# Kernel tuning notes

Measured on AMD Instinct MI355X. Metric: run time of the kernel, lower is better.

The kernel has to match this reference:

```python
import jax, jax.numpy as jnp
import numpy as np

Q, N, D = 4096, 100000, 128


def setup_inputs() -> dict:
    key = jax.random.key(0)
    k1, k2, k3 = jax.random.split(key, 3)
    inputs = jax.random.normal(k1, (Q, D), dtype=jnp.float32)
    X_train = jax.random.normal(k2, (N, D), dtype=jnp.float32)
    y_train = jax.random.normal(k3, (N,), dtype=jnp.float32)
    return {"inputs": inputs, "X_train": X_train, "y_train": y_train, "k": 32}


def reference(inputs, X_train, y_train, k):
    # Squared Euclidean distances [Q, N] via the expanded identity
    # |a-b|^2 = |a|^2 + |b|^2 - 2 a.b  (avoids materializing [Q, N, D]).
    q_sq = jnp.sum(inputs * inputs, axis=-1, keepdims=True)        # [Q, 1]
    t_sq = jnp.sum(X_train * X_train, axis=-1)                     # [N]
    cross = jnp.einsum('qd,nd->qn', inputs, X_train)               # [Q, N]
    distances = q_sq + t_sq[None, :] - 2.0 * cross                 # [Q, N]
    # top_k of -distances == k nearest neighbors
    _, indices = jax.lax.top_k(-distances, k)                      # [Q, k]
    nearest = y_train[indices]                                     # [Q, k]
    return jnp.mean(nearest, axis=1)                               # [Q]
```

## Files before the change

kernel.cpp:

```cpp
#include <hip/hip_runtime.h>
#include <hip/hip_fp16.h>
#include <cstdint>
#include <cstddef>


constexpr int Q_  = 4096;
constexpr int N_  = 100000;
constexpr int D_  = 128;
constexpr int K_  = 32;

constexpr int QT    = 16;
constexpr int BN    = 256;
constexpr int NCH   = 8;
constexpr int CHUNK = 12544;
constexpr int ITERS = CHUNK / BN;
constexpr int NPAD  = NCH * CHUNK;
constexpr int CW    = 128;
constexpr int QTS   = 16;
constexpr int SAMP_M      = 8192;
constexpr int SAMP_STRIDE = 12;
constexpr int SAMP_OFF    = 5;
constexpr int SAMP_ITERS  = SAMP_M / BN;

constexpr int XS_B  = NPAD / 64;
constexpr int SAM_B = SAMP_M / 64;
constexpr int PQ_B  = Q_ / 4;
constexpr int MXN   = XS_B * 4;

typedef __attribute__((ext_vector_type(8))) _Float16 half8;
typedef __attribute__((ext_vector_type(4))) float    floatx4;
typedef unsigned long long ull;

#define DEV __device__ __forceinline__
constexpr ull DEADC = ~0ull;

DEV ull pack_cand(float score, unsigned int n) {
    unsigned int s = __float_as_uint(score);
    s = (s & 0x80000000u) ? ~s : (s | 0x80000000u);
    return ((ull)s << 32) | (ull)n;
}
DEV float unpack_score(ull k) {
    unsigned int s = (unsigned int)(k >> 32);
    s = (s & 0x80000000u) ? (s ^ 0x80000000u) : ~s;
    return __uint_as_float(s);
}
DEV ull u64min(ull a, ull b) { return a < b ? a : b; }
DEV float inf_f() { return __int_as_float(0x7f800000); }

DEV ull bitonic64(ull v, int L) {
    #pragma unroll
    for (int k2 = 2; k2 <= 64; k2 <<= 1)
        #pragma unroll
        for (int j2 = k2 >> 1; j2 >= 1; j2 >>= 1) {
            ull o = __shfl_xor(v, j2);
            bool up = ((L & k2) == 0);
            bool lo = ((L & j2) == 0);
            ull mn = u64min(v, o), mx = v ^ o ^ mn;
            v = (lo == up) ? mn : mx;
        }
    return v;
}
DEV ull bimerge64(ull v, int L) {
    #pragma unroll
    for (int j2 = 32; j2 >= 1; j2 >>= 1) {
        ull o = __shfl_xor(v, j2);
        ull mn = u64min(v, o), mx = v ^ o ^ mn;
        v = ((L & j2) == 0) ? mn : mx;
    }
    return v;
}

__global__ void prep_all(const float* __restrict__ X, const float* __restrict__ Qm,
                         __half* __restrict__ Xs, float* __restrict__ tsq,
                         float* __restrict__ mxArr,
                         __half* __restrict__ Xsam, float* __restrict__ tsqS,
                         __half* __restrict__ Qh, __half* __restrict__ Qr,
                         float* __restrict__ qsq, int* __restrict__ flagF)
{
    const int tid = threadIdx.x, L = tid & 63, wv = tid >> 6;
    const int bx = blockIdx.x;
    const int am = L & 15, aq = L >> 4;

    if (bx < XS_B) {
        int t16 = bx * 4 + wv;
        int r = t16 * 16 + am;
        float ssq = 0.f, xr2 = 0.f;
        #pragma unroll
        for (int ks = 0; ks < 4; ++ks) {
            int c = ks * 32 + aq * 8;
            float v0=0,v1=0,v2=0,v3=0,v4=0,v5=0,v6=0,v7=0;
            if (r < N_) {
                float4 a = *(const float4*)(X + (size_t)r * D_ + c);
                float4 b = *(const float4*)(X + (size_t)r * D_ + c + 4);
                v0=a.x; v1=a.y; v2=a.z; v3=a.w; v4=b.x; v5=b.y; v6=b.z; v7=b.w;
            }
            half8 h;
            h[0]=(_Float16)v0; h[1]=(_Float16)v1; h[2]=(_Float16)v2; h[3]=(_Float16)v3;
            h[4]=(_Float16)v4; h[5]=(_Float16)v5; h[6]=(_Float16)v6; h[7]=(_Float16)v7;
            float r0=v0-(float)h[0], r1=v1-(float)h[1], r2=v2-(float)h[2], r3=v3-(float)h[3];
            float r4=v4-(float)h[4], r5=v5-(float)h[5], r6=v6-(float)h[6], r7=v7-(float)h[7];
            ssq += v0*v0+v1*v1+v2*v2+v3*v3+v4*v4+v5*v5+v6*v6+v7*v7;
            xr2 += r0*r0+r1*r1+r2*r2+r3*r3+r4*r4+r5*r5+r6*r6+r7*r7;
            *(half8*)(Xs + ((size_t)(t16 * 4 + ks)) * 512 + L * 8) = h;
        }
        ssq += __shfl_xor(ssq, 16); ssq += __shfl_xor(ssq, 32);
        xr2 += __shfl_xor(xr2, 16); xr2 += __shfl_xor(xr2, 32);
        if (aq == 0) tsq[r] = (r < N_) ? ssq : inf_f();
        float m = xr2;
        m = fmaxf(m, __shfl_xor(m, 1)); m = fmaxf(m, __shfl_xor(m, 2));
        m = fmaxf(m, __shfl_xor(m, 4)); m = fmaxf(m, __shfl_xor(m, 8));
        if (L == 0) mxArr[t16] = m;
    } else if (bx < XS_B + SAM_B) {
        int t16 = (bx - XS_B) * 4 + wv;
        int j = t16 * 16 + am;
        int n = j * SAMP_STRIDE + SAMP_OFF;
        float ssq = 0.f;
        #pragma unroll
        for (int ks = 0; ks < 4; ++ks) {
            int c = ks * 32 + aq * 8;
            float4 a = *(const float4*)(X + (size_t)n * D_ + c);
            float4 b = *(const float4*)(X + (size_t)n * D_ + c + 4);
            half8 h;
            h[0]=(_Float16)a.x; h[1]=(_Float16)a.y; h[2]=(_Float16)a.z; h[3]=(_Float16)a.w;
            h[4]=(_Float16)b.x; h[5]=(_Float16)b.y; h[6]=(_Float16)b.z; h[7]=(_Float16)b.w;
            ssq += a.x*a.x + a.y*a.y + a.z*a.z + a.w*a.w
                 + b.x*b.x + b.y*b.y + b.z*b.z + b.w*b.w;
            *(half8*)(Xsam + ((size_t)(t16 * 4 + ks)) * 512 + L * 8) = h;
        }
        ssq += __shfl_xor(ssq, 16); ssq += __shfl_xor(ssq, 32);
        if (aq == 0) tsqS[j] = ssq;
    } else {
        int r = (bx - XS_B - SAM_B) * 4 + wv;
        float2 x = *(const float2*)(Qm + (size_t)r * D_ + 2 * L);
        __half h0 = __float2half(x.x), h1 = __float2half(x.y);
        size_t o = (size_t)r * D_ + 2 * L;
        Qh[o] = h0; Qh[o + 1] = h1;
        Qr[o]     = __float2half(x.x - __half2float(h0));
        Qr[o + 1] = __float2half(x.y - __half2float(h1));
        float s = x.x * x.x + x.y * x.y;
        s += __shfl_xor(s, 32); s += __shfl_xor(s, 16); s += __shfl_xor(s, 8);
        s += __shfl_xor(s, 4);  s += __shfl_xor(s, 2);  s += __shfl_xor(s, 1);
        if (L == 0) { qsq[r] = s; flagF[r] = 0; }
    }
}

__global__ __launch_bounds__(256, 2) void sample_T(
    const __half* __restrict__ Qh, const __half* __restrict__ Qr,
    const __half* __restrict__ Xsam, const float* __restrict__ tsqS,
    const float* __restrict__ qsq, const float* __restrict__ mxArr,
    float* __restrict__ Teff, float* __restrict__ rawT, float* __restrict__ EwA)
{
    __shared__ float sT[QTS][130];
    const int tid = threadIdx.x, L = tid & 63, wv = tid >> 6;
    const int qbase = blockIdx.x * QTS;
    const int nwv = wv * 64;
    const int am = L & 15, aq = L >> 4;

    half8 afh[4], afr[4];
    #pragma unroll
    for (int ks = 0; ks < 4; ++ks) {
        size_t o = (size_t)(qbase + am) * D_ + ks * 32 + aq * 8;
        afh[ks] = *(const half8*)(Qh + o);
        afr[ks] = *(const half8*)(Qr + o);
    }

    float t2a[4], t2b[4];
    #pragma unroll
    for (int rg = 0; rg < 4; ++rg) { t2a[rg] = inf_f(); t2b[rg] = inf_f(); }

    const __half* bp = Xsam + (size_t)nwv * 128 + (size_t)L * 8;
    const float*  tp = tsqS + nwv + am;

    half8 bc[4], bn[4];
    #pragma unroll
    for (int nt = 0; nt < 4; ++nt)
        bc[nt] = *(const half8*)(bp + nt * 2048);

    #pragma unroll 1
    for (int it = 0; it < SAMP_ITERS; ++it) {
        float ts[4];
        #pragma unroll
        for (int nt = 0; nt < 4; ++nt) ts[nt] = tp[nt * 16];

        floatx4 acc[4] = {};
        #pragma unroll
        for (int ks = 0; ks < 4; ++ks) {
            const __half* pp = (ks < 3) ? (bp + (ks + 1) * 512) : (bp + 32768);
            #pragma unroll
            for (int nt = 0; nt < 4; ++nt)
                bn[nt] = *(const half8*)(pp + nt * 2048);
            #pragma unroll
            for (int nt = 0; nt < 4; ++nt) {
                acc[nt] = __builtin_amdgcn_mfma_f32_16x16x32_f16(
                    afh[ks], bc[nt], acc[nt], 0, 0, 0);
                acc[nt] = __builtin_amdgcn_mfma_f32_16x16x32_f16(
                    afr[ks], bc[nt], acc[nt], 0, 0, 0);
            }
            #pragma unroll
            for (int nt = 0; nt < 4; ++nt) bc[nt] = bn[nt];
        }
        #pragma unroll
        for (int rg = 0; rg < 4; ++rg) {
            float m1 = t2a[rg], m2 = t2b[rg];
            #pragma unroll
            for (int nt = 0; nt < 4; ++nt) {
                float v = ts[nt] - 2.f * acc[nt][rg];
                if (v < m2) { if (v < m1) { m2 = m1; m1 = v; } else m2 = v; }
            }
            t2a[rg] = m1; t2b[rg] = m2;
        }
        bp += 32768; tp += BN;
    }
    #pragma unroll
    for (int rg = 0; rg < 4; ++rg) {
        int q = aq * 4 + rg;
        sT[q][wv * 32 + am * 2 + 0] = t2a[rg];
        sT[q][wv * 32 + am * 2 + 1] = t2b[rg];
    }
    __syncthreads();

    float mxr = 0.f;
    #pragma unroll 1
    for (int i = L; i < MXN; i += 64) mxr = fmaxf(mxr, mxArr[i]);
    mxr = fmaxf(mxr, __shfl_xor(mxr, 32)); mxr = fmaxf(mxr, __shfl_xor(mxr, 16));
    mxr = fmaxf(mxr, __shfl_xor(mxr, 8));  mxr = fmaxf(mxr, __shfl_xor(mxr, 4));
    mxr = fmaxf(mxr, __shfl_xor(mxr, 2));  mxr = fmaxf(mxr, __shfl_xor(mxr, 1));

    #pragma unroll 1
    for (int j = 0; j < 4; ++j) {
        int q = wv * 4 + j;
        float a = sT[q][2 * L], b = sT[q][2 * L + 1];
        float g = 0.f;
        #pragma unroll 1
        for (int r = 0; r < 16; ++r) {
            float mn = fminf(a, b);
            mn = fminf(mn, __shfl_xor(mn, 32)); mn = fminf(mn, __shfl_xor(mn, 16));
            mn = fminf(mn, __shfl_xor(mn, 8));  mn = fminf(mn, __shfl_xor(mn, 4));
            mn = fminf(mn, __shfl_xor(mn, 2));  mn = fminf(mn, __shfl_xor(mn, 1));
            g = mn;
            ull ba = __ballot(a == g);
            if (ba) { if (L == __ffsll(ba) - 1) a = inf_f(); }
            else    { ull bb = __ballot(b == g); if (L == __ffsll(bb) - 1) b = inf_f(); }
        }
        if (L == 0) {
            int gq = qbase + q;
            float e = 2.f * sqrtf(qsq[gq]) * sqrtf(mxr) + 0.02f;
            rawT[gq] = g; EwA[gq] = e; Teff[gq] = g + e;
        }
    }
}

__global__ __launch_bounds__(256, 4) void knn_main(
    const __half* __restrict__ Qh, const __half* __restrict__ Qr,
    const __half* __restrict__ Xs, const float* __restrict__ tsq,
    const float* __restrict__ Teff, ull* __restrict__ candG,
    int* __restrict__ cntC, int* __restrict__ flagF)
{
    __shared__ ull candL[QT][CW];
    __shared__ int cntL[QT];

    const int tid = threadIdx.x, L = tid & 63, wv = tid >> 6;
    const int lb = blockIdx.x, ch = lb & 7;
    const int qbase = (lb >> 3) * QT, chBase = ch * CHUNK, nwv = wv * 64;
    const int am = L & 15, aq = L >> 4;

    if (tid < QT) cntL[tid] = 0;
    __syncthreads();

    float th[4];
    #pragma unroll
    for (int rg = 0; rg < 4; ++rg)
        th[rg] = Teff[qbase + aq * 4 + rg];
    float maxTh = fmaxf(fmaxf(th[0], th[1]), fmaxf(th[2], th[3]));
    const float negHalfMaxTh = -0.5f * maxTh - 1e-3f;

    half8 afh[4], afr[4];
    #pragma unroll
    for (int ks = 0; ks < 4; ++ks) {
        size_t o = (size_t)(qbase + am) * D_ + ks * 32 + aq * 8;
        afh[ks] = *(const half8*)(Qh + o);
        afr[ks] = *(const half8*)(Qr + o);
    }

    const __half* bp = Xs + (size_t)(chBase + nwv) * 128 + (size_t)L * 8;
    const float*  tp = tsq + chBase + nwv + am;
    int n0 = chBase + nwv + am;

    half8 bc[4], bn[4];
    #pragma unroll
    for (int nt = 0; nt < 4; ++nt)
        bc[nt] = *(const half8*)(bp + nt * 2048);

    #pragma unroll 1
    for (int it = 0; it < ITERS; ++it) {
        float ts[4];
        #pragma unroll
        for (int nt = 0; nt < 4; ++nt) ts[nt] = tp[nt * 16];

        floatx4 acc[4] = {};
        #pragma unroll
        for (int ks = 0; ks < 4; ++ks) {
            const __half* pp = (ks < 3) ? (bp + (ks + 1) * 512) : (bp + 32768);
            #pragma unroll
            for (int nt = 0; nt < 4; ++nt)
                bn[nt] = *(const half8*)(pp + nt * 2048);
            #pragma unroll
            for (int nt = 0; nt < 4; ++nt) {
                acc[nt] = __builtin_amdgcn_mfma_f32_16x16x32_f16(
                    afh[ks], bc[nt], acc[nt], 0, 0, 0);
                acc[nt] = __builtin_amdgcn_mfma_f32_16x16x32_f16(
                    afr[ks], bc[nt], acc[nt], 0, 0, 0);
            }
            #pragma unroll
            for (int nt = 0; nt < 4; ++nt) bc[nt] = bn[nt];
        }

        unsigned hit = 0;
        #pragma unroll
        for (int nt = 0; nt < 4; ++nt) {
            float mx = fmaxf(fmaxf(acc[nt][0], acc[nt][1]),
                             fmaxf(acc[nt][2], acc[nt][3]));
            float Gm = fmaf(0.5f, ts[nt], negHalfMaxTh);
            if (mx > Gm) hit |= 1u << nt;
        }
        if (__any(hit != 0)) {
            #pragma unroll
            for (int nt = 0; nt < 4; ++nt) {
                if (!__any(hit & (1u << nt))) continue;
                unsigned n = (unsigned)(n0 + nt * 16);
                #pragma unroll
                for (int rg = 0; rg < 4; ++rg) {
                    float s = fmaf(-2.f, acc[nt][rg], ts[nt]);
                    if (s < th[rg]) {
                        int q = aq * 4 + rg;
                        int pos = atomicAdd(&cntL[q], 1);
                        if (pos < CW)
                            candL[q][pos] = pack_cand(s, n);
                        else
                            flagF[qbase + q] = 1;
                    }
                }
            }
        }
        bp += 32768; tp += BN; n0 += BN;
    }

    __syncthreads();

    #pragma unroll 1
    for (int j = 0; j < 4; ++j) {
        int q = wv * 4 + j;
        int gq = qbase + q;
        int c = cntL[q];
        int cc = c < CW ? c : CW;
        ull* dst = candG + ((size_t)gq * NCH + ch) * CW;
        #pragma unroll
        for (int off = 0; off < CW; off += 64)
            if (off + L < cc) dst[off + L] = candL[q][off + L];
        if (L == 0) cntC[gq * NCH + ch] = cc;
    }
}

__global__ void finalize(const ull* __restrict__ candG, const int* __restrict__ cntC,
                         const int* __restrict__ flagF, const float* __restrict__ Qm,
                         const float* __restrict__ X, const float* __restrict__ tsq,
                         const float* __restrict__ rawT, const float* __restrict__ EwA,
                         const float* __restrict__ Ytr, float* __restrict__ out)
{
    __shared__ ull fb[4][256];
    int L = threadIdx.x & 63;
    int wv = threadIdx.x >> 6;
    int q = blockIdx.x * 4 + wv;
    bool bad = (flagF[q] != 0);
    float result = 0.f;

    if (!bad) {
        int cg = (L < NCH) ? cntC[q * NCH + L] : 0;
        int ctot = cg;
        ctot += __shfl_xor(ctot, 32); ctot += __shfl_xor(ctot, 16);
        ctot += __shfl_xor(ctot, 8);  ctot += __shfl_xor(ctot, 4);
        ctot += __shfl_xor(ctot, 2);  ctot += __shfl_xor(ctot, 1);
        if (ctot < K_) bad = true;
        else {
            ull s = DEADC;
            #pragma unroll 1
            for (int g = 0; g < NCH; ++g) {
                int c_g = __shfl(cg, g);
                const ull* cb = candG + ((size_t)q * NCH + g) * CW;
                #pragma unroll 1
                for (int off = 0; off < c_g; off += 64) {
                    ull v = (off + L < c_g) ? cb[off + L] : DEADC;
                    v = bitonic64(v, L);
                    ull w = __shfl(v, 63 - L);
                    s = bimerge64(u64min(s, w), L);
                }
            }
            int cr = ctot < 64 ? ctot : 64;
            unsigned n = (unsigned)(s & 0xffffffffu);
            ull pe = DEADC;
            if (L < cr) {
                const float4* xp = (const float4*)(X + (size_t)n * D_);
                const float4* qp = (const float4*)(Qm + (size_t)q * D_);
                float d = 0.f;
                #pragma unroll 8
                for (int i = 0; i < 32; ++i) {
                    float4 xv = xp[i], qv = qp[i];
                    d += qv.x * xv.x + qv.y * xv.y + qv.z * xv.z + qv.w * xv.w;
                }
                pe = pack_cand(tsq[n] - 2.f * d, n);
            }
            ull pe2 = bitonic64(pe, L);
            float exact31 = unpack_score(__shfl(pe2, K_ - 1));
            bool ok = exact31 < rawT[q];
            if (ctot > 64) {
                float A63 = unpack_score(__shfl(s, 63));
                ok = ok && (A63 - EwA[q] > exact31);
            }
            if (!ok) bad = true;
            else {
                float ys = 0.f;
                if (L < K_) ys = Ytr[(unsigned)(pe2 & 0xffffffffu)];
                ys += __shfl_xor(ys, 32); ys += __shfl_xor(ys, 16);
                ys += __shfl_xor(ys, 8);  ys += __shfl_xor(ys, 4);
                ys += __shfl_xor(ys, 2);  ys += __shfl_xor(ys, 1);
                result = ys * (1.f / K_);
            }
        }
    }

    if (bad) {
        const float4* qp = (const float4*)(Qm + (size_t)q * D_);
        float T = rawT[q] + EwA[q];
        float lo = 0.f, hi = 0.f;
        bool haveLo = false, haveHi = false;
        int cnt = 0;
        #pragma unroll 1
        for (int att = 0; att < 40; ++att) {
            cnt = 0;
            #pragma unroll 1
            for (int j = 0; j < NPAD / 64; ++j) {
                int n = j * 64 + L;
                float s = inf_f();
                if (n < N_) {
                    const float4* xp = (const float4*)(X + (size_t)n * D_);
                    float d = 0.f;
                    #pragma unroll 4
                    for (int i = 0; i < 32; ++i) {
                        float4 xv = xp[i], qv = qp[i];
                        d += qv.x * xv.x + qv.y * xv.y + qv.z * xv.z + qv.w * xv.w;
                    }
                    s = tsq[n] - 2.f * d;
                }
                bool want = s < T;
                ull m = __ballot(want);
                if (m) {
                    int pos = cnt + (int)__popcll(m & ((1ull << L) - 1ull));
                    if (want && pos < 256) fb[wv][pos] = pack_cand(s, (unsigned)n);
                    cnt += (int)__popcll(m);
                }
            }
            if (cnt >= K_ && cnt <= 256) break;
            if (cnt < K_) { lo = T; haveLo = true;
                T = haveHi ? 0.5f * (T + hi) : T + exp2f((float)att) * 0.5f; }
            else { hi = T; haveHi = true;
                T = haveLo ? 0.5f * (lo + T) : T - exp2f((float)att) * 0.5f; }
        }
        if (cnt >= K_ && cnt <= 256) {
            ull s64 = DEADC;
            #pragma unroll 1
            for (int off = 0; off < 256; off += 64) {
                if (off >= cnt) break;
                ull v = (off + L < cnt) ? fb[wv][off + L] : DEADC;
                v = bitonic64(v, L);
                ull w = __shfl(v, 63 - L);
                s64 = bimerge64(u64min(s64, w), L);
            }
            float ys = (L < K_) ? Ytr[(unsigned)(s64 & 0xffffffffu)] : 0.f;
            ys += __shfl_xor(ys, 32); ys += __shfl_xor(ys, 16);
            ys += __shfl_xor(ys, 8);  ys += __shfl_xor(ys, 4);
            ys += __shfl_xor(ys, 2);  ys += __shfl_xor(ys, 1);
            result = ys * (1.f / K_);
        } else {
            ull last = 0;
            float ysum = 0.f;
            for (int r = 0; r < K_; ++r) {
                ull best = DEADC;
                for (int j = 0; j < NPAD / 64; ++j) {
                    int n = j * 64 + L;
                    if (n < N_) {
                        const float4* xp = (const float4*)(X + (size_t)n * D_);
                        float d = 0.f;
                        #pragma unroll 4
                        for (int i = 0; i < 32; ++i) {
                            float4 xv = xp[i], qv = qp[i];
                            d += qv.x * xv.x + qv.y * xv.y + qv.z * xv.z + qv.w * xv.w;
                        }
                        ull k = pack_cand(tsq[n] - 2.f * d, n);
                        if (k > last && k < best) best = k;
                    }
                }
                best = u64min(best, __shfl_xor(best, 32));
                best = u64min(best, __shfl_xor(best, 16));
                best = u64min(best, __shfl_xor(best, 8));
                best = u64min(best, __shfl_xor(best, 4));
                best = u64min(best, __shfl_xor(best, 2));
                best = u64min(best, __shfl_xor(best, 1));
                if (L == 0) ysum += Ytr[(unsigned)(best & 0xffffffffu)];
                last = best;
            }
            result = ysum * (1.f / K_);
        }
    }
    if (L == 0) out[q] = result;
}

extern "C" void kernel_launch(void* const* d_in, const int* in_sizes, int n_in,
                              void* d_out, int out_size, void* d_ws, size_t ws_size,
                              hipStream_t stream)
{
    const float* Qm  = (const float*)d_in[0];
    const float* X   = (const float*)d_in[1];
    const float* Ytr = (const float*)d_in[2];
    float* out = (float*)d_out;

    char* w = (char*)d_ws;
    auto alloc = [&](size_t bytes) {
        char* p = w; w += (bytes + 255) & ~(size_t)255; return p;
    };
    __half* Xs   = (__half*)  alloc((size_t)(NPAD + BN) * D_ * 2);
    __half* Qh   = (__half*)  alloc((size_t)Q_ * D_ * 2);
    __half* Qr   = (__half*)  alloc((size_t)Q_ * D_ * 2);
    float*  ts   = (float*)   alloc((size_t)NPAD * 4);
    __half* Xsm  = (__half*)  alloc((size_t)(SAMP_M + BN) * D_ * 2);
    float*  tsS  = (float*)   alloc((size_t)SAMP_M * 4);
    ull*    cd   = (ull*)     alloc((size_t)Q_ * NCH * CW * 8);
    int*    cnC  = (int*)     alloc((size_t)Q_ * NCH * 4);
    int*    flg  = (int*)     alloc((size_t)Q_ * 4);
    float*  mxA  = (float*)   alloc((size_t)MXN * 4);
    float*  Tef  = (float*)   alloc((size_t)Q_ * 4);
    float*  rwT  = (float*)   alloc((size_t)Q_ * 4);
    float*  Ew   = (float*)   alloc((size_t)Q_ * 4);
    float*  qs   = (float*)   alloc((size_t)Q_ * 4);

    prep_all<<<XS_B + SAM_B + PQ_B, 256, 0, stream>>>(
        X, Qm, Xs, ts, mxA, Xsm, tsS, Qh, Qr, qs, flg);
    sample_T<<<Q_ / QTS, 256, 0, stream>>>(Qh, Qr, Xsm, tsS, qs, mxA, Tef, rwT, Ew);
    knn_main<<<(Q_ / QT) * NCH, 256, 0, stream>>>(Qh, Qr, Xs, ts, Tef, cd, cnC, flg);
    finalize<<<Q_ / 4, 256, 0, stream>>>(cd, cnC, flg, Qm, X, ts, rwT, Ew, Ytr, out);
}
```

Baseline: 481.3 us.

## Drop query residual MFMA, widen error bound, and tile two query groups per block

Removes the fp16 query-residual (Qr) MFMA pass from both the sampling and main filter kernels, halving matrix-core work per distance tile. To stay exact, the candidate threshold margin gains a term bounding the dropped query-residual contribution using the query residual norm and the maximum fp16-converted train-row norm. The freed work is used to process 32 queries per block (two 16-row A fragments sharing each loaded B fragment), which doubles reuse of the train tiles and halves the number of main blocks. The trade-off is a looser threshold, so more candidates reach the exact finalize stage and the per-query candidate buffer may overflow more often, plus more registers with occupancy lowered to 3 waves-per-SIMD bound.

```diff
diff --git a/kernel.cpp b/kernel.cpp
--- a/kernel.cpp
+++ b/kernel.cpp
@@ -9,7 +9,7 @@
 constexpr int D_  = 128;
 constexpr int K_  = 32;
 
-constexpr int QT    = 16;
+constexpr int QT    = 32;
 constexpr int BN    = 256;
 constexpr int NCH   = 8;
 constexpr int CHUNK = 12544;
@@ -72,10 +72,11 @@
 
 __global__ void prep_all(const float* __restrict__ X, const float* __restrict__ Qm,
                          __half* __restrict__ Xs, float* __restrict__ tsq,
-                         float* __restrict__ mxArr,
+                         float* __restrict__ mxArr, float* __restrict__ mxArrH,
                          __half* __restrict__ Xsam, float* __restrict__ tsqS,
-                         __half* __restrict__ Qh, __half* __restrict__ Qr,
-                         float* __restrict__ qsq, int* __restrict__ flagF)
+                         __half* __restrict__ Qh,
+                         float* __restrict__ qsq, float* __restrict__ qrs,
+                         int* __restrict__ flagF)
 {
     const int tid = threadIdx.x, L = tid & 63, wv = tid >> 6;
     const int bx = blockIdx.x;
@@ -84,7 +85,7 @@
     if (bx < XS_B) {
         int t16 = bx * 4 + wv;
         int r = t16 * 16 + am;
-        float ssq = 0.f, xr2 = 0.f;
+        float ssq = 0.f, xr2 = 0.f, xh2 = 0.f;
         #pragma unroll
         for (int ks = 0; ks < 4; ++ks) {
             int c = ks * 32 + aq * 8;
@@ -97,19 +98,26 @@
             half8 h;
             h[0]=(_Float16)v0; h[1]=(_Float16)v1; h[2]=(_Float16)v2; h[3]=(_Float16)v3;
             h[4]=(_Float16)v4; h[5]=(_Float16)v5; h[6]=(_Float16)v6; h[7]=(_Float16)v7;
-            float r0=v0-(float)h[0], r1=v1-(float)h[1], r2=v2-(float)h[2], r3=v3-(float)h[3];
-            float r4=v4-(float)h[4], r5=v5-(float)h[5], r6=v6-(float)h[6], r7=v7-(float)h[7];
+            float c0=(float)h[0], c1=(float)h[1], c2=(float)h[2], c3=(float)h[3];
+            float c4=(float)h[4], c5=(float)h[5], c6=(float)h[6], c7=(float)h[7];
+            float r0=v0-c0, r1=v1-c1, r2=v2-c2, r3=v3-c3;
+            float r4=v4-c4, r5=v5-c5, r6=v6-c6, r7=v7-c7;
             ssq += v0*v0+v1*v1+v2*v2+v3*v3+v4*v4+v5*v5+v6*v6+v7*v7;
             xr2 += r0*r0+r1*r1+r2*r2+r3*r3+r4*r4+r5*r5+r6*r6+r7*r7;
+            xh2 += c0*c0+c1*c1+c2*c2+c3*c3+c4*c4+c5*c5+c6*c6+c7*c7;
             *(half8*)(Xs + ((size_t)(t16 * 4 + ks)) * 512 + L * 8) = h;
         }
         ssq += __shfl_xor(ssq, 16); ssq += __shfl_xor(ssq, 32);
         xr2 += __shfl_xor(xr2, 16); xr2 += __shfl_xor(xr2, 32);
+        xh2 += __shfl_xor(xh2, 16); xh2 += __shfl_xor(xh2, 32);
         if (aq == 0) tsq[r] = (r < N_) ? ssq : inf_f();
         float m = xr2;
         m = fmaxf(m, __shfl_xor(m, 1)); m = fmaxf(m, __shfl_xor(m, 2));
         m = fmaxf(m, __shfl_xor(m, 4)); m = fmaxf(m, __shfl_xor(m, 8));
-        if (L == 0) mxArr[t16] = m;
+        float mh = xh2;
+        mh = fmaxf(mh, __shfl_xor(mh, 1)); mh = fmaxf(mh, __shfl_xor(mh, 2));
+        mh = fmaxf(mh, __shfl_xor(mh, 4)); mh = fmaxf(mh, __shfl_xor(mh, 8));
+        if (L == 0) { mxArr[t16] = m; mxArrH[t16] = mh; }
     } else if (bx < XS_B + SAM_B) {
         int t16 = (bx - XS_B) * 4 + wv;
         int j = t16 * 16 + am;
@@ -135,19 +143,22 @@
         __half h0 = __float2half(x.x), h1 = __float2half(x.y);
         size_t o = (size_t)r * D_ + 2 * L;
         Qh[o] = h0; Qh[o + 1] = h1;
-        Qr[o]     = __float2half(x.x - __half2float(h0));
-        Qr[o + 1] = __float2half(x.y - __half2float(h1));
-        float s = x.x * x.x + x.y * x.y;
-        s += __shfl_xor(s, 32); s += __shfl_xor(s, 16); s += __shfl_xor(s, 8);
-        s += __shfl_xor(s, 4);  s += __shfl_xor(s, 2);  s += __shfl_xor(s, 1);
-        if (L == 0) { qsq[r] = s; flagF[r] = 0; }
+        float r0 = x.x - __half2float(h0), r1 = x.y - __half2float(h1);
+        float s  = x.x * x.x + x.y * x.y;
+        float sr = r0 * r0 + r1 * r1;
+        s  += __shfl_xor(s, 32);  s += __shfl_xor(s, 16);  s += __shfl_xor(s, 8);
+        s  += __shfl_xor(s, 4);   s += __shfl_xor(s, 2);   s += __shfl_xor(s, 1);
+        sr += __shfl_xor(sr, 32); sr += __shfl_xor(sr, 16); sr += __shfl_xor(sr, 8);
+        sr += __shfl_xor(sr, 4);  sr += __shfl_xor(sr, 2);  sr += __shfl_xor(sr, 1);
+        if (L == 0) { qsq[r] = s; qrs[r] = sr; flagF[r] = 0; }
     }
 }
 
 __global__ __launch_bounds__(256, 2) void sample_T(
-    const __half* __restrict__ Qh, const __half* __restrict__ Qr,
-    const __half* __restrict__ Xsam, const float* __restrict__ tsqS,
-    const float* __restrict__ qsq, const float* __restrict__ mxArr,
+    const __half* __restrict__ Qh, const __half* __restrict__ Xsam,
+    const float* __restrict__ tsqS, const float* __restrict__ qsq,
+    const float* __restrict__ qrs, const float* __restrict__ mxArr,
+    const float* __restrict__ mxArrH,
     float* __restrict__ Teff, float* __restrict__ rawT, float* __restrict__ EwA)
 {
     __shared__ float sT[QTS][130];
@@ -156,12 +167,11 @@
     const int nwv = wv * 64;
     const int am = L & 15, aq = L >> 4;
 
-    half8 afh[4], afr[4];
+    half8 afh[4];
     #pragma unroll
     for (int ks = 0; ks < 4; ++ks) {
         size_t o = (size_t)(qbase + am) * D_ + ks * 32 + aq * 8;
         afh[ks] = *(const half8*)(Qh + o);
-        afr[ks] = *(const half8*)(Qr + o);
     }
 
     float t2a[4], t2b[4];
@@ -190,12 +200,9 @@
             for (int nt = 0; nt < 4; ++nt)
                 bn[nt] = *(const half8*)(pp + nt * 2048);
             #pragma unroll
-            for (int nt = 0; nt < 4; ++nt) {
+            for (int nt = 0; nt < 4; ++nt)
                 acc[nt] = __builtin_amdgcn_mfma_f32_16x16x32_f16(
                     afh[ks], bc[nt], acc[nt], 0, 0, 0);
-                acc[nt] = __builtin_amdgcn_mfma_f32_16x16x32_f16(
-                    afr[ks], bc[nt], acc[nt], 0, 0, 0);
-            }
             #pragma unroll
             for (int nt = 0; nt < 4; ++nt) bc[nt] = bn[nt];
         }
@@ -219,12 +226,18 @@
     }
     __syncthreads();
 
-    float mxr = 0.f;
+    float mxr = 0.f, mxh = 0.f;
     #pragma unroll 1
-    for (int i = L; i < MXN; i += 64) mxr = fmaxf(mxr, mxArr[i]);
+    for (int i = L; i < MXN; i += 64) {
+        mxr = fmaxf(mxr, mxArr[i]);
+        mxh = fmaxf(mxh, mxArrH[i]);
+    }
     mxr = fmaxf(mxr, __shfl_xor(mxr, 32)); mxr = fmaxf(mxr, __shfl_xor(mxr, 16));
     mxr = fmaxf(mxr, __shfl_xor(mxr, 8));  mxr = fmaxf(mxr, __shfl_xor(mxr, 4));
     mxr = fmaxf(mxr, __shfl_xor(mxr, 2));  mxr = fmaxf(mxr, __shfl_xor(mxr, 1));
+    mxh = fmaxf(mxh, __shfl_xor(mxh, 32)); mxh = fmaxf(mxh, __shfl_xor(mxh, 16));
+    mxh = fmaxf(mxh, __shfl_xor(mxh, 8));  mxh = fmaxf(mxh, __shfl_xor(mxh, 4));
+    mxh = fmaxf(mxh, __shfl_xor(mxh, 2));  mxh = fmaxf(mxh, __shfl_xor(mxh, 1));
 
     #pragma unroll 1
     for (int j = 0; j < 4; ++j) {
@@ -244,17 +257,17 @@
         }
         if (L == 0) {
             int gq = qbase + q;
-            float e = 2.f * sqrtf(qsq[gq]) * sqrtf(mxr) + 0.02f;
+            float e = 2.f * (sqrtf(qsq[gq]) * sqrtf(mxr)
+                           + sqrtf(qrs[gq]) * sqrtf(mxh)) + 0.02f;
             rawT[gq] = g; EwA[gq] = e; Teff[gq] = g + e;
         }
     }
 }
 
-__global__ __launch_bounds__(256, 4) void knn_main(
-    const __half* __restrict__ Qh, const __half* __restrict__ Qr,
-    const __half* __restrict__ Xs, const float* __restrict__ tsq,
-    const float* __restrict__ Teff, ull* __restrict__ candG,
-    int* __restrict__ cntC, int* __restrict__ flagF)
+__global__ __launch_bounds__(256, 3) void knn_main(
+    const __half* __restrict__ Qh, const __half* __restrict__ Xs,
+    const float* __restrict__ tsq, const float* __restrict__ Teff,
+    ull* __restrict__ candG, int* __restrict__ cntC, int* __restrict__ flagF)
 {
     __shared__ ull candL[QT][CW];
     __shared__ int cntL[QT];
@@ -267,20 +280,25 @@
     if (tid < QT) cntL[tid] = 0;
     __syncthreads();
 
-    float th[4];
-    #pragma unroll
-    for (int rg = 0; rg < 4; ++rg)
-        th[rg] = Teff[qbase + aq * 4 + rg];
-    float maxTh = fmaxf(fmaxf(th[0], th[1]), fmaxf(th[2], th[3]));
-    const float negHalfMaxTh = -0.5f * maxTh - 1e-3f;
-
-    half8 afh[4], afr[4];
-    #pragma unroll
-    for (int ks = 0; ks < 4; ++ks) {
-        size_t o = (size_t)(qbase + am) * D_ + ks * 32 + aq * 8;
-        afh[ks] = *(const half8*)(Qh + o);
-        afr[ks] = *(const half8*)(Qr + o);
-    }
+    float th[2][4];
+    float nH[2];
+    #pragma unroll
+    for (int qt = 0; qt < 2; ++qt) {
+        #pragma unroll
+        for (int rg = 0; rg < 4; ++rg)
+            th[qt][rg] = Teff[qbase + qt * 16 + aq * 4 + rg];
+        float m = fmaxf(fmaxf(th[qt][0], th[qt][1]), fmaxf(th[qt][2], th[qt][3]));
+        nH[qt] = -0.5f * m - 1e-3f;
+    }
+
+    half8 afh[2][4];
+    #pragma unroll
+    for (int qt = 0; qt < 2; ++qt)
+        #pragma unroll
+        for (int ks = 0; ks < 4; ++ks) {
+            size_t o = (size_t)(qbase + qt * 16 + am) * D_ + ks * 32 + aq * 8;
+            afh[qt][ks] = *(const half8*)(Qh + o);
+        }
 
     const __half* bp = Xs + (size_t)(chBase + nwv) * 128 + (size_t)L * 8;
     const float*  tp = tsq + chBase + nwv + am;
@@ -297,7 +315,7 @@
         #pragma unroll
         for (int nt = 0; nt < 4; ++nt) ts[nt] = tp[nt * 16];
 
-        floatx4 acc[4] = {};
+        floatx4 acc[2][4] = {};
         #pragma unroll
         for (int ks = 0; ks < 4; ++ks) {
             const __half* pp = (ks < 3) ? (bp + (ks + 1) * 512) : (bp + 32768);
@@ -306,10 +324,10 @@
                 bn[nt] = *(const half8*)(pp + nt * 2048);
             #pragma unroll
             for (int nt = 0; nt < 4; ++nt) {
-                acc[nt] = __builtin_amdgcn_mfma_f32_16x16x32_f16(
-                    afh[ks], bc[nt], acc[nt], 0, 0, 0);
-                acc[nt] = __builtin_amdgcn_mfma_f32_16x16x32_f16(
-                    afr[ks], bc[nt], acc[nt], 0, 0, 0);
+                acc[0][nt] = __builtin_amdgcn_mfma_f32_16x16x32_f16(
+                    afh[0][ks], bc[nt], acc[0][nt], 0, 0, 0);
+                acc[1][nt] = __builtin_amdgcn_mfma_f32_16x16x32_f16(
+                    afh[1][ks], bc[nt], acc[1][nt], 0, 0, 0);
             }
             #pragma unroll
             for (int nt = 0; nt < 4; ++nt) bc[nt] = bn[nt];
@@ -318,26 +336,32 @@
         unsigned hit = 0;
         #pragma unroll
         for (int nt = 0; nt < 4; ++nt) {
-            float mx = fmaxf(fmaxf(acc[nt][0], acc[nt][1]),
-                             fmaxf(acc[nt][2], acc[nt][3]));
-            float Gm = fmaf(0.5f, ts[nt], negHalfMaxTh);
-            if (mx > Gm) hit |= 1u << nt;
+            #pragma unroll
+            for (int qt = 0; qt < 2; ++qt) {
+                float mx = fmaxf(fmaxf(acc[qt][nt][0], acc[qt][nt][1]),
+                                 fmaxf(acc[qt][nt][2], acc[qt][nt][3]));
+                float Gm = fmaf(0.5f, ts[nt], nH[qt]);
+                if (mx > Gm) hit |= 1u << (nt * 2 + qt);
+            }
         }
         if (__any(hit != 0)) {
             #pragma unroll
             for (int nt = 0; nt < 4; ++nt) {
-                if (!__any(hit & (1u << nt))) continue;
-                unsigned n = (unsigned)(n0 + nt * 16);
                 #pragma unroll
-                for (int rg = 0; rg < 4; ++rg) {
-                    float s = fmaf(-2.f, acc[nt][rg], ts[nt]);
-                    if (s < th[rg]) {
-                        int q = aq * 4 + rg;
-                        int pos = atomicAdd(&cntL[q], 1);
-                        if (pos < CW)
-                            candL[q][pos] = pack_cand(s, n);
-                        else
-                            flagF[qbase + q] = 1;
+                for (int qt = 0; qt < 2; ++qt) {
+                    if (!__any(hit & (1u << (nt * 2 + qt)))) continue;
+                    unsigned n = (unsigned)(n0 + nt * 16);
+                    #pragma unroll
+                    for (int rg = 0; rg < 4; ++rg) {
+                        float s = fmaf(-2.f, acc[qt][nt][rg], ts[nt]);
+                        if (s < th[qt][rg]) {
+                            int q = qt * 16 + aq * 4 + rg;
+                            int pos = atomicAdd(&cntL[q], 1);
+                            if (pos < CW)
+                                candL[q][pos] = pack_cand(s, n);
+                            else
+                                flagF[qbase + q] = 1;
+                        }
                     }
                 }
             }
@@ -348,8 +372,8 @@
     __syncthreads();
 
     #pragma unroll 1
-    for (int j = 0; j < 4; ++j) {
-        int q = wv * 4 + j;
+    for (int j = 0; j < 8; ++j) {
+        int q = wv * 8 + j;
         int gq = qbase + q;
         int c = cntL[q];
         int cc = c < CW ? c : CW;
@@ -529,7 +553,6 @@
     };
     __half* Xs   = (__half*)  alloc((size_t)(NPAD + BN) * D_ * 2);
     __half* Qh   = (__half*)  alloc((size_t)Q_ * D_ * 2);
-    __half* Qr   = (__half*)  alloc((size_t)Q_ * D_ * 2);
     float*  ts   = (float*)   alloc((size_t)NPAD * 4);
     __half* Xsm  = (__half*)  alloc((size_t)(SAMP_M + BN) * D_ * 2);
     float*  tsS  = (float*)   alloc((size_t)SAMP_M * 4);
@@ -537,14 +560,17 @@
     int*    cnC  = (int*)     alloc((size_t)Q_ * NCH * 4);
     int*    flg  = (int*)     alloc((size_t)Q_ * 4);
     float*  mxA  = (float*)   alloc((size_t)MXN * 4);
+    float*  mxAH = (float*)   alloc((size_t)MXN * 4);
     float*  Tef  = (float*)   alloc((size_t)Q_ * 4);
     float*  rwT  = (float*)   alloc((size_t)Q_ * 4);
     float*  Ew   = (float*)   alloc((size_t)Q_ * 4);
     float*  qs   = (float*)   alloc((size_t)Q_ * 4);
+    float*  qr2  = (float*)   alloc((size_t)Q_ * 4);
 
     prep_all<<<XS_B + SAM_B + PQ_B, 256, 0, stream>>>(
-        X, Qm, Xs, ts, mxA, Xsm, tsS, Qh, Qr, qs, flg);
-    sample_T<<<Q_ / QTS, 256, 0, stream>>>(Qh, Qr, Xsm, tsS, qs, mxA, Tef, rwT, Ew);
-    knn_main<<<(Q_ / QT) * NCH, 256, 0, stream>>>(Qh, Qr, Xs, ts, Tef, cd, cnC, flg);
+        X, Qm, Xs, ts, mxA, mxAH, Xsm, tsS, Qh, qs, qr2, flg);
+    sample_T<<<Q_ / QTS, 256, 0, stream>>>(Qh, Xsm, tsS, qs, qr2, mxA, mxAH,
+                                           Tef, rwT, Ew);
+    knn_main<<<(Q_ / QT) * NCH, 256, 0, stream>>>(Qh, Xs, ts, Tef, cd, cnC, flg);
     finalize<<<Q_ / 4, 256, 0, stream>>>(cd, cnC, flg, Qm, X, ts, rwT, Ew, Ytr, out);
 }
```

Measured after the change: 436.6 us. -9.3%, faster.
